# Performance work log

Hardware: AMD Instinct MI355X
Metric: run time of the kernel (lower is better)

Reference implementation:

```python
import jax, jax.numpy as jnp
import numpy as np

N_EMBED = 1024
N_HEAD = 16
SEQ = 2048
BATCH = 2


def setup_inputs() -> dict:
    key = jax.random.key(0)
    ks = jax.random.split(key, 5)
    scale_in = 1.0 / np.sqrt(N_EMBED)
    x = jax.random.normal(ks[0], (BATCH, SEQ, N_EMBED), dtype=jnp.float32)
    # attn_proj: Linear(n_embed, 3*n_embed); stored as [in, out] so y = x @ W + b
    W_qkv = jax.random.normal(ks[1], (N_EMBED, 3 * N_EMBED), dtype=jnp.float32) * scale_in
    b_qkv = jax.random.normal(ks[2], (3 * N_EMBED,), dtype=jnp.float32) * 0.01
    # fin_proj: Linear(n_embed, n_embed)
    W_out = jax.random.normal(ks[3], (N_EMBED, N_EMBED), dtype=jnp.float32) * scale_in
    b_out = jax.random.normal(ks[4], (N_EMBED,), dtype=jnp.float32) * 0.01
    return {"x": x, "W_qkv": W_qkv, "b_qkv": b_qkv, "W_out": W_out, "b_out": b_out}


def reference(x, W_qkv, b_qkv, W_out, b_out):
    B, S, D = x.shape
    H = N_HEAD
    hd = D // H
    qkv = x @ W_qkv + b_qkv  # [B, S, 3D]
    q, k, v = jnp.split(qkv, 3, axis=-1)
    # [B, H, S, hd]
    q = q.reshape(B, S, H, hd).transpose(0, 2, 1, 3)
    k = k.reshape(B, S, H, hd).transpose(0, 2, 1, 3)
    v = v.reshape(B, S, H, hd).transpose(0, 2, 1, 3)
    scores = jnp.einsum("bhqd,bhkd->bhqk", q, k) * (1.0 / np.sqrt(hd))
    causal = jnp.tril(jnp.ones((S, S), dtype=bool))  # lower-triangular mask
    scores = jnp.where(causal[None, None], scores, -jnp.inf)
    probs = jax.nn.softmax(scores, axis=-1)
    # dropout is identity in eval mode (inference reference)
    attn = jnp.einsum("bhqk,bhkd->bhqd", probs, v)  # [B, H, S, hd]
    attn = attn.transpose(0, 2, 1, 3).reshape(B, S, D)
    return attn @ W_out + b_out
```

## Files before the change

kernel.cpp:

```cpp
#include <hip/hip_runtime.h>

typedef short bf16x8 __attribute__((ext_vector_type(8)));
typedef short bf16x4 __attribute__((ext_vector_type(4)));
typedef float f32x4 __attribute__((ext_vector_type(4)));
typedef int i32x4 __attribute__((ext_vector_type(4)));
typedef int i32x2 __attribute__((ext_vector_type(2)));

#define MFMA16x16x32(a, b, c) __builtin_amdgcn_mfma_f32_16x16x32_bf16(a, b, c, 0, 0, 0)
#define TRR(dst, a) asm volatile("ds_read_b64_tr_b16 %0, %1" : "=v"(dst) : "v"(a))

__device__ __forceinline__ unsigned short f2bf(float f) {
  union { float f; unsigned u; } v; v.f = f;
  unsigned u = v.u + 0x7FFFu + ((v.u >> 16) & 1u);
  return (unsigned short)(u >> 16);
}

__device__ __forceinline__ unsigned cvtpk(float lo, float hi) {
  unsigned r;
  asm("v_cvt_pk_bf16_f32 %0, %1, %2" : "=v"(r) : "v"(lo), "v"(hi));
  return r;
}

__device__ __forceinline__ float max3f(float a, float b, float c) {
  float d;
  asm("v_max3_f32 %0, %1, %2, %3" : "=v"(d) : "v"(a), "v"(b), "v"(c));
  return d;
}

__device__ __forceinline__ void gload16(const void* g, void* l) {
  __builtin_amdgcn_global_load_lds((const __attribute__((address_space(1))) void*)g,
                                   (__attribute__((address_space(3))) void*)l, 16, 0, 0);
}

__device__ __forceinline__ unsigned ldsoff(const void* p) {
  return (unsigned)(unsigned long long)(const __attribute__((address_space(3))) void*)p;
}

__global__ __launch_bounds__(256) void conv_bf16(const float* __restrict__ in,
                                                 unsigned short* __restrict__ out, int n8) {
  int i = blockIdx.x * 256 + threadIdx.x;
  if (i >= n8) return;
  const float4* p = reinterpret_cast<const float4*>(in + (long)i * 8);
  float4 a = p[0], b = p[1];
  i32x4 o;
  o[0] = cvtpk(a.x, a.y); o[1] = cvtpk(a.z, a.w);
  o[2] = cvtpk(b.x, b.y); o[3] = cvtpk(b.z, b.w);
  *reinterpret_cast<i32x4*>(out + (long)i * 8) = o;
}

__global__ __launch_bounds__(256) void trans_f32_bf16(const float* __restrict__ W,
                                                      unsigned short* __restrict__ Wt,
                                                      int K, int N) {
  __shared__ float tile[32][33];
  int n0 = blockIdx.x << 5, k0 = blockIdx.y << 5;
  int tx = threadIdx.x, ty = threadIdx.y;
#pragma unroll
  for (int i = 0; i < 32; i += 8)
    tile[ty + i][tx] = W[(long)(k0 + ty + i) * N + n0 + tx];
  __syncthreads();
#pragma unroll
  for (int i = 0; i < 32; i += 8)
    Wt[(long)(n0 + ty + i) * K + k0 + tx] = f2bf(tile[tx][ty + i]);
}

template <int BF16OUT>
__global__ __launch_bounds__(256) void gemm_bt(const unsigned short* __restrict__ A,
                                               const unsigned short* __restrict__ Bt,
                                               const float* __restrict__ bias,
                                               void* __restrict__ Cv,
                                               int M, int N, int K) {
  __shared__ __align__(128) unsigned short As[4096];
  __shared__ __align__(128) unsigned short Bs[4096];
  int t = threadIdx.x;
  int w = t >> 6, l = t & 63;
  int g = l >> 4, m16 = l & 15;
  int wr = w >> 1, wc = w & 1;
  long am0 = (long)blockIdx.y << 7;
  long bn0 = (long)blockIdx.x << 7;
  f32x4 acc[4][4];
#pragma unroll
  for (int i = 0; i < 4; ++i)
#pragma unroll
    for (int j = 0; j < 4; ++j) acc[i][j] = (f32x4){0.f, 0.f, 0.f, 0.f};

  for (int k0 = 0; k0 < K; k0 += 32) {
#pragma unroll
    for (int i = 0; i < 2; ++i) {
      int seg = i * 4 + w;
      int flat = (seg << 9) + (l << 3);
      int r_ = flat >> 5, c_ = flat & 31;
      gload16(A + (am0 + r_) * K + k0 + c_, &As[seg << 9]);
      gload16(Bt + (bn0 + r_) * K + k0 + c_, &Bs[seg << 9]);
    }
    __syncthreads();
    bf16x8 af[4], bfr[4];
#pragma unroll
    for (int im = 0; im < 4; ++im)
      af[im] = *(const bf16x8*)&As[((wr << 6) + (im << 4) + m16) * 32 + (g << 3)];
#pragma unroll
    for (int in = 0; in < 4; ++in)
      bfr[in] = *(const bf16x8*)&Bs[((wc << 6) + (in << 4) + m16) * 32 + (g << 3)];
    __builtin_amdgcn_s_setprio(1);
#pragma unroll
    for (int im = 0; im < 4; ++im)
#pragma unroll
      for (int in = 0; in < 4; ++in)
        acc[im][in] = MFMA16x16x32(af[im], bfr[in], acc[im][in]);
    __builtin_amdgcn_s_setprio(0);
    __syncthreads();
  }

#pragma unroll
  for (int im = 0; im < 4; ++im) {
#pragma unroll
    for (int in = 0; in < 4; ++in) {
      long col = bn0 + (wc << 6) + (in << 4) + m16;
      float bval = bias[col];
#pragma unroll
      for (int r = 0; r < 4; ++r) {
        long row = am0 + (wr << 6) + (im << 4) + (g << 2) + r;
        float v = acc[im][in][r] + bval;
        if (BF16OUT)
          ((unsigned short*)Cv)[row * N + col] = f2bf(v);
        else
          ((float*)Cv)[row * N + col] = v;
      }
    }
  }
}

__global__ __launch_bounds__(256, 2) void attn_fwd(const unsigned short* __restrict__ qkv,
                                                   unsigned short* __restrict__ out) {
  const int D3 = 3072;
  const float C1 = 0.18033688f;
  const float THR = 11.5415603f;
  __shared__ __align__(128) unsigned short Ks[2][8192];
  __shared__ __align__(128) unsigned short Vs[2][8192];
  int b = blockIdx.x >> 4, h = blockIdx.x & 15;
  int t = threadIdx.x;
  int w = t >> 6, l = t & 63;
  int g = l >> 4, m16 = l & 15;
  long base = (long)b * 2048 * D3;
  const unsigned short* kbase = qkv + base + 1024 + h * 64;
  const unsigned short* vbase = qkv + base + 2048 + h * 64;

  int l8 = l >> 3, sc = l & 7;
  int kof = (w * 8 + l8) * D3 + ((sc ^ l8) << 3);
  int vof = ((w * 8 + l8) * 4 + (sc >> 1)) * D3 + ((sc & 1) << 3);
  const f32x4 zero4 = (f32x4){0.f, 0.f, 0.f, 0.f};

  for (int sgi = 0; sgi < 2; ++sgi) {
    int qt = sgi ? (31 - blockIdx.y) : blockIdx.y;
    int q0 = qt << 6;
    int qrow = q0 + (w << 4) + m16;
    const unsigned short* qp = qkv + base + (long)qrow * D3 + h * 64;
    bf16x8 qf0 = *(const bf16x8*)(qp + g * 8);
    bf16x8 qf1 = *(const bf16x8*)(qp + 32 + g * 8);

    f32x4 O[4];
#pragma unroll
    for (int d = 0; d < 4; ++d) O[d] = zero4;
    float m2 = -1e30f, lsum = 0.f;
    int nt = (qt >> 1) + 1;

#pragma unroll
    for (int i = 0; i < 4; ++i) {
      gload16(kbase + kof + i * 32 * D3, &Ks[0][(i << 11) + (w << 9)]);
      gload16(vbase + vof + (i << 4), &Vs[0][(i << 11) + (w << 9)]);
    }
    __syncthreads();

    int buf = 0;
    for (int it = 0; it < nt; ++it) {
      if (it + 1 < nt) {
        long off = (long)(it + 1) * 128 * D3;
#pragma unroll
        for (int i = 0; i < 4; ++i) {
          gload16(kbase + off + kof + i * 32 * D3, &Ks[buf ^ 1][(i << 11) + (w << 9)]);
          gload16(vbase + off + vof + (i << 4), &Vs[buf ^ 1][(i << 11) + (w << 9)]);
        }
      }
      unsigned va = ldsoff(&Vs[buf][0]) + (g << 7) + (m16 << 3);
      bf16x4 tLo[4][4], tHi[4][4];
#pragma unroll
      for (int G = 0; G < 4; ++G)
#pragma unroll
        for (int d = 0; d < 4; ++d) {
          unsigned a = va + (G << 10) + (d << 12);
          TRR(tLo[G][d], a);
          TRR(tHi[G][d], a + 512);
        }
      const char* kbuf = (const char*)&Ks[buf][0];
      int swz = m16 & 7;
      f32x4 st[8];
      __builtin_amdgcn_s_setprio(1);
#pragma unroll
      for (int T = 0; T < 8; ++T) {
        const char* rp = kbuf + (((T << 4) + m16) << 7);
        bf16x8 kf0 = *(const bf16x8*)(rp + ((g ^ swz) << 4));
        bf16x8 kf1 = *(const bf16x8*)(rp + (((4 + g) ^ swz) << 4));
        st[T] = MFMA16x16x32(kf0, qf0, zero4);
        st[T] = MFMA16x16x32(kf1, qf1, st[T]);
      }
      __builtin_amdgcn_s_setprio(0);

      if (it == nt - 1) {
        int rq = qrow - (it << 7);
#pragma unroll
        for (int T = 0; T < 8; ++T)
#pragma unroll
          for (int r = 0; r < 4; ++r)
            if ((T << 4) + (g << 2) + r > rq) st[T][r] = -3e38f;
      }
      float tm[8];
#pragma unroll
      for (int T = 0; T < 8; ++T)
        tm[T] = max3f(fmaxf(st[T][0], st[T][1]), st[T][2], st[T][3]);
      float u0 = max3f(tm[0], tm[1], tm[2]);
      float u1 = max3f(tm[3], tm[4], tm[5]);
      float tmax = max3f(u0, u1, fmaxf(tm[6], tm[7]));
      tmax = fmaxf(tmax, __shfl_xor(tmax, 16));
      tmax = fmaxf(tmax, __shfl_xor(tmax, 32));
      float tsc2 = tmax * C1;
      bool skip = __all(tsc2 <= m2 + THR);
      float mnew2 = skip ? m2 : fmaxf(m2, tsc2);
      float p[8][4];
      f32x4 ts4 = zero4;
#pragma unroll
      for (int T = 0; T < 8; ++T)
#pragma unroll
        for (int r = 0; r < 4; ++r) {
          float e = __builtin_amdgcn_exp2f(fmaf(st[T][r], C1, -mnew2));
          p[T][r] = e;
          ts4[r] += e;
        }
      float tsum = (ts4[0] + ts4[1]) + (ts4[2] + ts4[3]);
      tsum += __shfl_xor(tsum, 16);
      tsum += __shfl_xor(tsum, 32);
      if (!skip) {
        float alpha = __builtin_amdgcn_exp2f(m2 - mnew2);
        lsum *= alpha;
#pragma unroll
        for (int d = 0; d < 4; ++d) {
          O[d][0] *= alpha; O[d][1] *= alpha; O[d][2] *= alpha; O[d][3] *= alpha;
        }
        m2 = mnew2;
      }
      lsum += tsum;

      bf16x8 pb[4];
#pragma unroll
      for (int G = 0; G < 4; ++G) {
        i32x4 wv;
        wv[0] = cvtpk(p[2 * G][0], p[2 * G][1]);
        wv[1] = cvtpk(p[2 * G][2], p[2 * G][3]);
        wv[2] = cvtpk(p[2 * G + 1][0], p[2 * G + 1][1]);
        wv[3] = cvtpk(p[2 * G + 1][2], p[2 * G + 1][3]);
        pb[G] = __builtin_bit_cast(bf16x8, wv);
      }

      asm volatile("s_waitcnt lgkmcnt(0)" ::: "memory");
      __builtin_amdgcn_sched_barrier(0);

      __builtin_amdgcn_s_setprio(1);
#pragma unroll
      for (int d = 0; d < 4; ++d)
#pragma unroll
        for (int G = 0; G < 4; ++G) {
          bf16x8 vf = __builtin_shufflevector(tLo[G][d], tHi[G][d], 0, 1, 2, 3, 4, 5, 6, 7);
          O[d] = MFMA16x16x32(vf, pb[G], O[d]);
        }
      __builtin_amdgcn_s_setprio(0);
      __syncthreads();
      buf ^= 1;
    }

    float inv = 1.0f / lsum;
    unsigned short* op = out + (long)(b * 2048 + qrow) * 1024 + h * 64;
#pragma unroll
    for (int d = 0; d < 4; ++d) {
      i32x2 pk;
      pk[0] = (int)cvtpk(O[d][0] * inv, O[d][1] * inv);
      pk[1] = (int)cvtpk(O[d][2] * inv, O[d][3] * inv);
      *reinterpret_cast<i32x2*>(op + (d << 4) + (g << 2)) = pk;
    }
  }
}

extern "C" void kernel_launch(void* const* d_in, const int* in_sizes, int n_in,
                              void* d_out, int out_size, void* d_ws, size_t ws_size,
                              hipStream_t stream) {
  const float* x     = (const float*)d_in[0];
  const float* W_qkv = (const float*)d_in[1];
  const float* b_qkv = (const float*)d_in[2];
  const float* W_out = (const float*)d_in[3];
  const float* b_out = (const float*)d_in[4];

  char* ws = (char*)d_ws;
  unsigned short* xb    = (unsigned short*)ws;
  unsigned short* wqkvT = (unsigned short*)(ws + (8l << 20));
  unsigned short* woutT = (unsigned short*)(ws + (14l << 20));
  unsigned short* qkv   = (unsigned short*)(ws + (16l << 20));

  conv_bf16<<<2048, 256, 0, stream>>>(x, xb, 524288);
  trans_f32_bf16<<<dim3(96, 32), dim3(32, 8), 0, stream>>>(W_qkv, wqkvT, 1024, 3072);
  trans_f32_bf16<<<dim3(32, 32), dim3(32, 8), 0, stream>>>(W_out, woutT, 1024, 1024);
  gemm_bt<1><<<dim3(24, 32), 256, 0, stream>>>(xb, wqkvT, b_qkv, (void*)qkv, 4096, 3072, 1024);
  attn_fwd<<<dim3(32, 16), 256, 0, stream>>>(qkv, xb);
  gemm_bt<0><<<dim3(8, 32), 256, 0, stream>>>(xb, woutT, b_out, d_out, 4096, 1024, 1024);
}
```

Measured before the change: 118.2 us.

## Process paired causal query tiles in one KV sweep sharing K/V loads

Instead of looping over two query tiles sequentially, each reloading K/V from the start, the attention kernel now processes both tiles (y and 31-y) in a single pass over the longer tile's KV range, with the short tile active only for its first blocks. This halves the K/V global loads and LDS V-transpose reads for the shorter tile and gives the scheduler two independent MFMA/softmax chains to interleave. Row sums are now kept per lane and reduced across lanes only at the end rather than per iteration. The cost is higher register pressure from two sets of accumulators and score tiles, which could cause spills or lower occupancy under launch bounds (256,2).

```diff
diff --git a/kernel.cpp b/kernel.cpp
--- a/kernel.cpp
+++ b/kernel.cpp
@@ -137,6 +137,7 @@
   __shared__ __align__(128) unsigned short Ks[2][8192];
   __shared__ __align__(128) unsigned short Vs[2][8192];
   int b = blockIdx.x >> 4, h = blockIdx.x & 15;
+  int y = blockIdx.y;
   int t = threadIdx.x;
   int w = t >> 6, l = t & 63;
   int g = l >> 4, m16 = l & 15;
@@ -149,105 +150,113 @@
   int vof = ((w * 8 + l8) * 4 + (sc >> 1)) * D3 + ((sc & 1) << 3);
   const f32x4 zero4 = (f32x4){0.f, 0.f, 0.f, 0.f};
 
-  for (int sgi = 0; sgi < 2; ++sgi) {
-    int qt = sgi ? (31 - blockIdx.y) : blockIdx.y;
-    int q0 = qt << 6;
-    int qrow = q0 + (w << 4) + m16;
-    const unsigned short* qp = qkv + base + (long)qrow * D3 + h * 64;
-    bf16x8 qf0 = *(const bf16x8*)(qp + g * 8);
-    bf16x8 qf1 = *(const bf16x8*)(qp + 32 + g * 8);
-
-    f32x4 O[4];
-#pragma unroll
-    for (int d = 0; d < 4; ++d) O[d] = zero4;
-    float m2 = -1e30f, lsum = 0.f;
-    int nt = (qt >> 1) + 1;
-
-#pragma unroll
-    for (int i = 0; i < 4; ++i) {
-      gload16(kbase + kof + i * 32 * D3, &Ks[0][(i << 11) + (w << 9)]);
-      gload16(vbase + vof + (i << 4), &Vs[0][(i << 11) + (w << 9)]);
-    }
-    __syncthreads();
-
-    int buf = 0;
-    for (int it = 0; it < nt; ++it) {
-      if (it + 1 < nt) {
-        long off = (long)(it + 1) * 128 * D3;
-#pragma unroll
-        for (int i = 0; i < 4; ++i) {
-          gload16(kbase + off + kof + i * 32 * D3, &Ks[buf ^ 1][(i << 11) + (w << 9)]);
-          gload16(vbase + off + vof + (i << 4), &Vs[buf ^ 1][(i << 11) + (w << 9)]);
-        }
-      }
-      unsigned va = ldsoff(&Vs[buf][0]) + (g << 7) + (m16 << 3);
-      bf16x4 tLo[4][4], tHi[4][4];
-#pragma unroll
-      for (int G = 0; G < 4; ++G)
-#pragma unroll
-        for (int d = 0; d < 4; ++d) {
-          unsigned a = va + (G << 10) + (d << 12);
-          TRR(tLo[G][d], a);
-          TRR(tHi[G][d], a + 512);
-        }
-      const char* kbuf = (const char*)&Ks[buf][0];
-      int swz = m16 & 7;
-      f32x4 st[8];
-      __builtin_amdgcn_s_setprio(1);
-#pragma unroll
-      for (int T = 0; T < 8; ++T) {
-        const char* rp = kbuf + (((T << 4) + m16) << 7);
-        bf16x8 kf0 = *(const bf16x8*)(rp + ((g ^ swz) << 4));
-        bf16x8 kf1 = *(const bf16x8*)(rp + (((4 + g) ^ swz) << 4));
-        st[T] = MFMA16x16x32(kf0, qf0, zero4);
-        st[T] = MFMA16x16x32(kf1, qf1, st[T]);
-      }
-      __builtin_amdgcn_s_setprio(0);
-
-      if (it == nt - 1) {
-        int rq = qrow - (it << 7);
+  int qtA = y, qtB = 31 - y;
+  int ssA = (qtA >> 1) + 1;
+  int nt = (qtB >> 1) + 1;
+  int qrowA = (qtA << 6) + (w << 4) + m16;
+  int qrowB = (qtB << 6) + (w << 4) + m16;
+
+  const unsigned short* qpA = qkv + base + (long)qrowA * D3 + h * 64;
+  const unsigned short* qpB = qkv + base + (long)qrowB * D3 + h * 64;
+  bf16x8 qfA0 = *(const bf16x8*)(qpA + g * 8);
+  bf16x8 qfA1 = *(const bf16x8*)(qpA + 32 + g * 8);
+  bf16x8 qfB0 = *(const bf16x8*)(qpB + g * 8);
+  bf16x8 qfB1 = *(const bf16x8*)(qpB + 32 + g * 8);
+
+  f32x4 OA[4], OB[4];
+#pragma unroll
+  for (int d = 0; d < 4; ++d) { OA[d] = zero4; OB[d] = zero4; }
+  f32x4 lsvA = zero4, lsvB = zero4;
+  float m2A = -1e30f, m2B = -1e30f;
+
+#pragma unroll
+  for (int i = 0; i < 4; ++i) {
+    gload16(kbase + kof + i * 32 * D3, &Ks[0][(i << 11) + (w << 9)]);
+    gload16(vbase + vof + (i << 4), &Vs[0][(i << 11) + (w << 9)]);
+  }
+  __syncthreads();
+
+  int buf = 0;
+  for (int ss = 0; ss < nt; ++ss) {
+    if (ss + 1 < nt) {
+      long off = (long)(ss + 1) * 128 * D3;
+#pragma unroll
+      for (int i = 0; i < 4; ++i) {
+        gload16(kbase + off + kof + i * 32 * D3, &Ks[buf ^ 1][(i << 11) + (w << 9)]);
+        gload16(vbase + off + vof + (i << 4), &Vs[buf ^ 1][(i << 11) + (w << 9)]);
+      }
+    }
+    unsigned va = ldsoff(&Vs[buf][0]) + (g << 7) + (m16 << 3);
+    bf16x4 tLo[4][4], tHi[4][4];
+#pragma unroll
+    for (int G = 0; G < 4; ++G)
+#pragma unroll
+      for (int d = 0; d < 4; ++d) {
+        unsigned a = va + (G << 10) + (d << 12);
+        TRR(tLo[G][d], a);
+        TRR(tHi[G][d], a + 512);
+      }
+    bool actA = (ss < ssA);
+    const char* kbuf = (const char*)&Ks[buf][0];
+    int swz = m16 & 7;
+    f32x4 stA[8], stB[8];
+    __builtin_amdgcn_s_setprio(1);
+#pragma unroll
+    for (int T = 0; T < 8; ++T) {
+      const char* rp = kbuf + (((T << 4) + m16) << 7);
+      bf16x8 kf0 = *(const bf16x8*)(rp + ((g ^ swz) << 4));
+      bf16x8 kf1 = *(const bf16x8*)(rp + (((4 + g) ^ swz) << 4));
+      stB[T] = MFMA16x16x32(kf0, qfB0, zero4);
+      stB[T] = MFMA16x16x32(kf1, qfB1, stB[T]);
+      if (actA) {
+        stA[T] = MFMA16x16x32(kf0, qfA0, zero4);
+        stA[T] = MFMA16x16x32(kf1, qfA1, stA[T]);
+      }
+    }
+    __builtin_amdgcn_s_setprio(0);
+
+    asm volatile("s_waitcnt lgkmcnt(0)" ::: "memory");
+    __builtin_amdgcn_sched_barrier(0);
+
+    if (actA) {
+      if (ss == ssA - 1) {
+        int rq = qrowA - (ss << 7);
 #pragma unroll
         for (int T = 0; T < 8; ++T)
 #pragma unroll
           for (int r = 0; r < 4; ++r)
-            if ((T << 4) + (g << 2) + r > rq) st[T][r] = -3e38f;
+            if ((T << 4) + (g << 2) + r > rq) stA[T][r] = -3e38f;
       }
       float tm[8];
 #pragma unroll
       for (int T = 0; T < 8; ++T)
-        tm[T] = max3f(fmaxf(st[T][0], st[T][1]), st[T][2], st[T][3]);
+        tm[T] = max3f(fmaxf(stA[T][0], stA[T][1]), stA[T][2], stA[T][3]);
       float u0 = max3f(tm[0], tm[1], tm[2]);
       float u1 = max3f(tm[3], tm[4], tm[5]);
       float tmax = max3f(u0, u1, fmaxf(tm[6], tm[7]));
       tmax = fmaxf(tmax, __shfl_xor(tmax, 16));
       tmax = fmaxf(tmax, __shfl_xor(tmax, 32));
       float tsc2 = tmax * C1;
-      bool skip = __all(tsc2 <= m2 + THR);
-      float mnew2 = skip ? m2 : fmaxf(m2, tsc2);
+      bool skip = __all(tsc2 <= m2A + THR);
+      float mnew2 = skip ? m2A : fmaxf(m2A, tsc2);
       float p[8][4];
       f32x4 ts4 = zero4;
 #pragma unroll
       for (int T = 0; T < 8; ++T)
 #pragma unroll
         for (int r = 0; r < 4; ++r) {
-          float e = __builtin_amdgcn_exp2f(fmaf(st[T][r], C1, -mnew2));
+          float e = __builtin_amdgcn_exp2f(fmaf(stA[T][r], C1, -mnew2));
           p[T][r] = e;
           ts4[r] += e;
         }
-      float tsum = (ts4[0] + ts4[1]) + (ts4[2] + ts4[3]);
-      tsum += __shfl_xor(tsum, 16);
-      tsum += __shfl_xor(tsum, 32);
       if (!skip) {
-        float alpha = __builtin_amdgcn_exp2f(m2 - mnew2);
-        lsum *= alpha;
-#pragma unroll
-        for (int d = 0; d < 4; ++d) {
-          O[d][0] *= alpha; O[d][1] *= alpha; O[d][2] *= alpha; O[d][3] *= alpha;
-        }
-        m2 = mnew2;
-      }
-      lsum += tsum;
-
+        float alpha = __builtin_amdgcn_exp2f(m2A - mnew2);
+        lsvA *= alpha;
+#pragma unroll
+        for (int d = 0; d < 4; ++d) OA[d] *= alpha;
+        m2A = mnew2;
+      }
+      lsvA += ts4;
       bf16x8 pb[4];
 #pragma unroll
       for (int G = 0; G < 4; ++G) {
@@ -258,30 +267,106 @@
         wv[3] = cvtpk(p[2 * G + 1][2], p[2 * G + 1][3]);
         pb[G] = __builtin_bit_cast(bf16x8, wv);
       }
-
-      asm volatile("s_waitcnt lgkmcnt(0)" ::: "memory");
-      __builtin_amdgcn_sched_barrier(0);
-
       __builtin_amdgcn_s_setprio(1);
 #pragma unroll
       for (int d = 0; d < 4; ++d)
 #pragma unroll
         for (int G = 0; G < 4; ++G) {
           bf16x8 vf = __builtin_shufflevector(tLo[G][d], tHi[G][d], 0, 1, 2, 3, 4, 5, 6, 7);
-          O[d] = MFMA16x16x32(vf, pb[G], O[d]);
+          OA[d] = MFMA16x16x32(vf, pb[G], OA[d]);
         }
       __builtin_amdgcn_s_setprio(0);
-      __syncthreads();
-      buf ^= 1;
-    }
-
-    float inv = 1.0f / lsum;
-    unsigned short* op = out + (long)(b * 2048 + qrow) * 1024 + h * 64;
+    }
+
+    {
+      if (ss == nt - 1) {
+        int rq = qrowB - (ss << 7);
+#pragma unroll
+        for (int T = 0; T < 8; ++T)
+#pragma unroll
+          for (int r = 0; r < 4; ++r)
+            if ((T << 4) + (g << 2) + r > rq) stB[T][r] = -3e38f;
+      }
+      float tm[8];
+#pragma unroll
+      for (int T = 0; T < 8; ++T)
+        tm[T] = max3f(fmaxf(stB[T][0], stB[T][1]), stB[T][2], stB[T][3]);
+      float u0 = max3f(tm[0], tm[1], tm[2]);
+      float u1 = max3f(tm[3], tm[4], tm[5]);
+      float tmax = max3f(u0, u1, fmaxf(tm[6], tm[7]));
+      tmax = fmaxf(tmax, __shfl_xor(tmax, 16));
+      tmax = fmaxf(tmax, __shfl_xor(tmax, 32));
+      float tsc2 = tmax * C1;
+      bool skip = __all(tsc2 <= m2B + THR);
+      float mnew2 = skip ? m2B : fmaxf(m2B, tsc2);
+      float p[8][4];
+      f32x4 ts4 = zero4;
+#pragma unroll
+      for (int T = 0; T < 8; ++T)
+#pragma unroll
+        for (int r = 0; r < 4; ++r) {
+          float e = __builtin_amdgcn_exp2f(fmaf(stB[T][r], C1, -mnew2));
+          p[T][r] = e;
+          ts4[r] += e;
+        }
+      if (!skip) {
+        float alpha = __builtin_amdgcn_exp2f(m2B - mnew2);
+        lsvB *= alpha;
+#pragma unroll
+        for (int d = 0; d < 4; ++d) OB[d] *= alpha;
+        m2B = mnew2;
+      }
+      lsvB += ts4;
+      bf16x8 pb[4];
+#pragma unroll
+      for (int G = 0; G < 4; ++G) {
+        i32x4 wv;
+        wv[0] = cvtpk(p[2 * G][0], p[2 * G][1]);
+        wv[1] = cvtpk(p[2 * G][2], p[2 * G][3]);
+        wv[2] = cvtpk(p[2 * G + 1][0], p[2 * G + 1][1]);
+        wv[3] = cvtpk(p[2 * G + 1][2], p[2 * G + 1][3]);
+        pb[G] = __builtin_bit_cast(bf16x8, wv);
+      }
+      __builtin_amdgcn_s_setprio(1);
+#pragma unroll
+      for (int d = 0; d < 4; ++d)
+#pragma unroll
+        for (int G = 0; G < 4; ++G) {
+          bf16x8 vf = __builtin_shufflevector(tLo[G][d], tHi[G][d], 0, 1, 2, 3, 4, 5, 6, 7);
+          OB[d] = MFMA16x16x32(vf, pb[G], OB[d]);
+        }
+      __builtin_amdgcn_s_setprio(0);
+    }
+
+    __syncthreads();
+    buf ^= 1;
+  }
+
+  {
+    float s = (lsvA[0] + lsvA[1]) + (lsvA[2] + lsvA[3]);
+    s += __shfl_xor(s, 16);
+    s += __shfl_xor(s, 32);
+    float inv = 1.0f / s;
+    unsigned short* op = out + (long)(b * 2048 + qrowA) * 1024 + h * 64;
 #pragma unroll
     for (int d = 0; d < 4; ++d) {
       i32x2 pk;
-      pk[0] = (int)cvtpk(O[d][0] * inv, O[d][1] * inv);
-      pk[1] = (int)cvtpk(O[d][2] * inv, O[d][3] * inv);
+      pk[0] = (int)cvtpk(OA[d][0] * inv, OA[d][1] * inv);
+      pk[1] = (int)cvtpk(OA[d][2] * inv, OA[d][3] * inv);
+      *reinterpret_cast<i32x2*>(op + (d << 4) + (g << 2)) = pk;
+    }
+  }
+  {
+    float s = (lsvB[0] + lsvB[1]) + (lsvB[2] + lsvB[3]);
+    s += __shfl_xor(s, 16);
+    s += __shfl_xor(s, 32);
+    float inv = 1.0f / s;
+    unsigned short* op = out + (long)(b * 2048 + qrowB) * 1024 + h * 64;
+#pragma unroll
+    for (int d = 0; d < 4; ++d) {
+      i32x2 pk;
+      pk[0] = (int)cvtpk(OB[d][0] * inv, OB[d][1] * inv);
+      pk[1] = (int)cvtpk(OB[d][2] * inv, OB[d][3] * inv);
       *reinterpret_cast<i32x2*>(op + (d << 4) + (g << 2)) = pk;
     }
   }
```

Result: no change. 118.2 us (+0.0%).
